# Kernel optimization log

Measured on AMD Instinct MI355X. Metric: run time of the kernel, lower is better.

Reference implementation:

```python
import jax, jax.numpy as jnp
import numpy as np

B, S, DIN = 1, 2048, 4096
H, KV, DH = 32, 8, 128          # num_heads, num_kv_groups, head_dim
G = H // KV                      # group_size


def setup_inputs() -> dict:
    key = jax.random.key(0)
    ks = jax.random.split(key, 6)
    input_tensor = jax.random.normal(ks[0], (B, S, DIN), jnp.float32)
    # boolean mask: True = masked out. Causal upper-triangular mask.
    attention_mask = jnp.triu(jnp.ones((S, S), bool), k=1)[None, None]
    # RoPE tables (context_len, head_dim), rotate-half layout
    inv_freq = 1.0 / (10000.0 ** (jnp.arange(0, DH, 2, dtype=jnp.float32) / DH))
    ang = jnp.arange(S, dtype=jnp.float32)[:, None] * inv_freq[None, :]  # (S, DH/2)
    ang = jnp.concatenate([ang, ang], axis=-1)                            # (S, DH)
    cos, sin = jnp.cos(ang), jnp.sin(ang)
    scale = 0.02
    Wq = jax.random.normal(ks[1], (DIN, H * DH), jnp.float32) * scale
    Wk = jax.random.normal(ks[2], (DIN, KV * DH), jnp.float32) * scale
    Wv = jax.random.normal(ks[3], (DIN, KV * DH), jnp.float32) * scale
    Wo = jax.random.normal(ks[4], (H * DH, DIN), jnp.float32) * scale
    return {"input_tensor": input_tensor, "attention_mask": attention_mask,
            "cos": cos, "sin": sin, "Wq": Wq, "Wk": Wk, "Wv": Wv, "Wo": Wo}


def _rope(t, cos, sin):
    # t: (B, heads, S, DH); cos/sin: (S, DH)
    t1, t2 = jnp.split(t, 2, axis=-1)
    rot = jnp.concatenate([-t2, t1], axis=-1)
    return t * cos[None, None] + rot * sin[None, None]


def reference(input_tensor, attention_mask, cos, sin, Wq, Wk, Wv, Wo):
    b, s, _ = input_tensor.shape
    q = (input_tensor @ Wq).reshape(b, s, H, DH).transpose(0, 2, 1, 3)   # (B,H,S,DH)
    k = (input_tensor @ Wk).reshape(b, s, KV, DH).transpose(0, 2, 1, 3)  # (B,KV,S,DH)
    v = (input_tensor @ Wv).reshape(b, s, KV, DH).transpose(0, 2, 1, 3)
    q = _rope(q, cos, sin)
    k = _rope(k, cos, sin)
    # GQA: duplicate each kv head across its group of query heads
    k = jnp.repeat(k, G, axis=1)  # (B,H,S,DH)
    v = jnp.repeat(v, G, axis=1)
    scores = jnp.einsum('bhqd,bhkd->bhqk', q, k)
    scores = jnp.where(attention_mask, -jnp.inf, scores)
    weights = jax.nn.softmax(scores / np.float32(np.sqrt(DH)), axis=-1)
    ctx = jnp.einsum('bhqk,bhkd->bhqd', weights, v)
    ctx = ctx.transpose(0, 2, 1, 3).reshape(b, s, H * DH)
    return ctx @ Wo
```

## Files before the change

kernel.cpp:

```cpp
#include <hip/hip_runtime.h>
#include <hip/hip_bf16.h>
#include <stdint.h>
#include <stddef.h>

typedef __attribute__((ext_vector_type(8))) short bf16x8;
typedef __attribute__((ext_vector_type(8))) unsigned short u16x8;
typedef __attribute__((ext_vector_type(4))) float f32x4;
typedef __attribute__((ext_vector_type(16))) float f32x16;

#define MFMA16(a, b, c) __builtin_amdgcn_mfma_f32_16x16x32_bf16((a), (b), (c), 0, 0, 0)
#define MFMA32(a, b, c) __builtin_amdgcn_mfma_f32_32x32x16_bf16((a), (b), (c), 0, 0, 0)

__device__ __forceinline__ unsigned short f2b(float f) {
  union { float f; unsigned u; } v; v.f = f;
  unsigned r = v.u + 0x7fffu + ((v.u >> 16) & 1u);
  return (unsigned short)(r >> 16);
}
__device__ __forceinline__ float b2f(unsigned short h) {
  union { unsigned u; float f; } v; v.u = ((unsigned)h) << 16;
  return v.f;
}

__device__ __forceinline__ void gload_lds16(const void* g, void* l) {
  __builtin_amdgcn_global_load_lds((const __attribute__((address_space(1))) void*)g,
                                   (__attribute__((address_space(3))) void*)l, 16, 0, 0);
}

__global__ void k_transpose_qkv(const float* __restrict__ Wq, const float* __restrict__ Wk,
                                const float* __restrict__ Wv, unsigned short* __restrict__ out) {
  __shared__ float tile[64][65];
  const int kb = blockIdx.x * 64;
  const int nbg = blockIdx.y * 64;
  const float* src; int srcN, nb;
  if (nbg < 4096)      { src = Wq; srcN = 4096; nb = nbg; }
  else if (nbg < 5120) { src = Wk; srcN = 1024; nb = nbg - 4096; }
  else                 { src = Wv; srcN = 1024; nb = nbg - 5120; }
  const int t = threadIdx.x;
  const int c4 = (t & 15) * 4;
  const int rr = t >> 4;
#pragma unroll
  for (int i = 0; i < 4; ++i) {
    int r = rr + i * 16;
    float4 v = *reinterpret_cast<const float4*>(src + (size_t)(kb + r) * srcN + nb + c4);
    tile[r][c4 + 0] = v.x; tile[r][c4 + 1] = v.y;
    tile[r][c4 + 2] = v.z; tile[r][c4 + 3] = v.w;
  }
  __syncthreads();
#pragma unroll
  for (int i = 0; i < 4; ++i) {
    int n = rr + i * 16;
    ushort4 w;
    w.x = f2b(tile[c4 + 0][n]); w.y = f2b(tile[c4 + 1][n]);
    w.z = f2b(tile[c4 + 2][n]); w.w = f2b(tile[c4 + 3][n]);
    *reinterpret_cast<ushort4*>(out + (size_t)(nbg + n) * 4096 + kb + c4) = w;
  }
}

__global__ void k_transpose_f32_bf16(const float* __restrict__ in,
                                     unsigned short* __restrict__ out,
                                     int K, int N) {
  __shared__ float tile[64][65];
  const int kb = blockIdx.x * 64;
  const int nb = blockIdx.y * 64;
  const int t = threadIdx.x;
  const int c4 = (t & 15) * 4;
  const int rr = t >> 4;
#pragma unroll
  for (int i = 0; i < 4; ++i) {
    int r = rr + i * 16;
    float4 v = *reinterpret_cast<const float4*>(in + (size_t)(kb + r) * N + nb + c4);
    tile[r][c4 + 0] = v.x; tile[r][c4 + 1] = v.y;
    tile[r][c4 + 2] = v.z; tile[r][c4 + 3] = v.w;
  }
  __syncthreads();
#pragma unroll
  for (int i = 0; i < 4; ++i) {
    int n = rr + i * 16;
    ushort4 w;
    w.x = f2b(tile[c4 + 0][n]); w.y = f2b(tile[c4 + 1][n]);
    w.z = f2b(tile[c4 + 2][n]); w.w = f2b(tile[c4 + 3][n]);
    *reinterpret_cast<ushort4*>(out + (size_t)(nb + n) * K + kb + c4) = w;
  }
}

__global__ void k_f32_to_bf16(const float* __restrict__ in, unsigned short* __restrict__ out) {
  size_t i = ((size_t)blockIdx.x * blockDim.x + threadIdx.x) * 4;
  float4 v = *reinterpret_cast<const float4*>(in + i);
  ushort4 w; w.x = f2b(v.x); w.y = f2b(v.y); w.z = f2b(v.z); w.w = f2b(v.w);
  *reinterpret_cast<ushort4*>(out + i) = w;
}

template <bool OUT_F32>
__global__ void __launch_bounds__(256, 2)
k_gemm(const unsigned short* __restrict__ A, const unsigned short* __restrict__ Bt,
       void* __restrict__ C, int M, int N, int K) {
  __shared__ unsigned short As[128 * 64];
  __shared__ unsigned short Bs[128 * 64];
  const int nbm = M >> 7;
  const int per = ((M >> 7) * (N >> 7)) >> 3;
  const int wg  = (blockIdx.x & 7) * per + (blockIdx.x >> 3);
  const int m0 = (wg % nbm) * 128;
  const int n0 = (wg / nbm) * 128;
  const int tid = threadIdx.x;
  const int lane = tid & 63;
  const int w = tid >> 6;
  const int wr = w >> 1, wc = w & 1;
  const int cl = lane & 15, rg = lane >> 4;

  f32x4 acc[4][4] = {};

  for (int k0 = 0; k0 < K; k0 += 64) {
#pragma unroll
    for (int i = 0; i < 4; ++i) {
      int c = i * 256 + tid;
      int row = c >> 3;
      int sc = ((c & 7) * 8) ^ ((row & 7) * 8);
      gload_lds16(A + (size_t)(m0 + row) * K + k0 + sc, As + c * 8);
    }
#pragma unroll
    for (int i = 0; i < 4; ++i) {
      int c = i * 256 + tid;
      int row = c >> 3;
      int sc = ((c & 7) * 8) ^ ((row & 7) * 8);
      gload_lds16(Bt + (size_t)(n0 + row) * K + k0 + sc, Bs + c * 8);
    }
    __syncthreads();
    bf16x8 a[4][2], b[4][2];
#pragma unroll
    for (int mi = 0; mi < 4; ++mi) {
      int row = wr * 64 + mi * 16 + cl;
      int swz = (row & 7) << 4;
#pragma unroll
      for (int ks = 0; ks < 2; ++ks)
        a[mi][ks] = *reinterpret_cast<const bf16x8*>(
            (const char*)As + ((row * 128 + (ks * 32 + rg * 8) * 2) ^ swz));
    }
#pragma unroll
    for (int ni = 0; ni < 4; ++ni) {
      int row = wc * 64 + ni * 16 + cl;
      int swz = (row & 7) << 4;
#pragma unroll
      for (int ks = 0; ks < 2; ++ks)
        b[ni][ks] = *reinterpret_cast<const bf16x8*>(
            (const char*)Bs + ((row * 128 + (ks * 32 + rg * 8) * 2) ^ swz));
    }
#pragma unroll
    for (int ks = 0; ks < 2; ++ks)
#pragma unroll
      for (int mi = 0; mi < 4; ++mi)
#pragma unroll
        for (int ni = 0; ni < 4; ++ni)
          acc[mi][ni] = MFMA16(a[mi][ks], b[ni][ks], acc[mi][ni]);
    __syncthreads();
  }
#pragma unroll
  for (int mi = 0; mi < 4; ++mi)
#pragma unroll
    for (int ni = 0; ni < 4; ++ni) {
      int row = m0 + wr * 64 + mi * 16 + rg * 4;
      int col = n0 + wc * 64 + ni * 16 + cl;
#pragma unroll
      for (int r = 0; r < 4; ++r) {
        float v = acc[mi][ni][r];
        if (OUT_F32) ((float*)C)[(size_t)(row + r) * N + col] = v;
        else         ((unsigned short*)C)[(size_t)(row + r) * N + col] = f2b(v);
      }
    }
}

__global__ void k_rope(const unsigned short* __restrict__ Cpre,
                       const float* __restrict__ cosb, const float* __restrict__ sinb,
                       unsigned short* __restrict__ Qr, unsigned short* __restrict__ Kr) {
  const int s = blockIdx.x;
  const int hh = blockIdx.y * 2 + (threadIdx.x >> 7);
  const int d = threadIdx.x & 127;
  const int col = (hh < 32) ? hh * 128 + d : 4096 + (hh - 32) * 128 + d;
  float t = b2f(Cpre[(size_t)s * 6144 + col]);
  const int dp = (d < 64) ? d + 64 : d - 64;
  float tp = b2f(Cpre[(size_t)s * 6144 + (col - d + dp)]);
  float rot = (d < 64) ? -tp : tp;
  float o = t * cosb[s * 128 + d] + rot * sinb[s * 128 + d];
  if (hh < 32) {
    Qr[((size_t)hh * 2048 + s) * 128 + d] = f2b(o * 0.08838834764831845f);
  } else {
    Kr[((size_t)(hh - 32) * 2048 + s) * 128 + d] = f2b(o);
  }
}

__global__ void k_transpose_v(const unsigned short* __restrict__ Cpre,
                              unsigned short* __restrict__ Vt) {
  __shared__ unsigned short tile[64][72];
  const int sb = blockIdx.x * 64;
  const int db = blockIdx.y * 64;
  const int kv = blockIdx.z;
  const int t = threadIdx.x;
#pragma unroll
  for (int i = 0; i < 2; ++i) {
    int sl = i * 32 + (t >> 3);
    int d8 = (t & 7) * 8;
    const unsigned short* src = Cpre + (size_t)(sb + sl) * 6144 + 5120 + kv * 128 + db + d8;
    ushort4 v0 = *reinterpret_cast<const ushort4*>(src);
    ushort4 v1 = *reinterpret_cast<const ushort4*>(src + 4);
    *reinterpret_cast<ushort4*>(&tile[sl][d8]) = v0;
    *reinterpret_cast<ushort4*>(&tile[sl][d8 + 4]) = v1;
  }
  __syncthreads();
#pragma unroll
  for (int i = 0; i < 2; ++i) {
    int dl = i * 32 + (t >> 3);
    int s8 = (t & 7) * 8;
    ushort4 w0, w1;
    w0.x = tile[s8 + 0][dl]; w0.y = tile[s8 + 1][dl]; w0.z = tile[s8 + 2][dl]; w0.w = tile[s8 + 3][dl];
    w1.x = tile[s8 + 4][dl]; w1.y = tile[s8 + 5][dl]; w1.z = tile[s8 + 6][dl]; w1.w = tile[s8 + 7][dl];
    unsigned short* dst = Vt + ((size_t)kv * 128 + db + dl) * 2048 + sb + s8;
    *reinterpret_cast<ushort4*>(dst) = w0;
    *reinterpret_cast<ushort4*>(dst + 4) = w1;
  }
}

__global__ void __launch_bounds__(256, 2)
k_attn(const unsigned short* __restrict__ Qr, const unsigned short* __restrict__ Kr,
       const unsigned short* __restrict__ Vt, unsigned short* __restrict__ ctx) {
  __shared__ unsigned short Ks[2][64 * 128];
  __shared__ unsigned short Vs[2][128 * 64];
  const int bid = blockIdx.x;
  const int kv = bid & 7;
  const int hd = kv * 4 + ((bid >> 3) & 3);
  const int qb = 15 - (bid >> 5);
  const int q0 = qb * 128;
  const int tid = threadIdx.x;
  const int l = tid & 63;
  const int w = tid >> 6;
  const int i5 = l & 31;
  const int h  = l >> 5;
  const int qg = q0 + w * 16 + (i5 & 15) + (i5 >> 4) * 64;

  const char* Kbase = (const char*)(Kr + (size_t)kv * 2048 * 128);
  const char* Vbase = (const char*)(Vt + (size_t)kv * 128 * 2048);

  bf16x8 qf[8];
#pragma unroll
  for (int s = 0; s < 8; ++s)
    qf[s] = *reinterpret_cast<const bf16x8*>(
        Qr + ((size_t)hd * 2048 + qg) * 128 + s * 16 + h * 8);

  f32x16 po[4] = {};
  float mrow = -1e30f, lrow = 0.f;

  const int krow = tid >> 4;
  const int kcol = (tid & 15) * 16;
  const int vrow = tid >> 3;
  const int vcol = (tid & 7) * 16;

#define STAGE_KV(JT, BUF)                                                      \
  {                                                                            \
    _Pragma("unroll")                                                          \
    for (int ii = 0; ii < 4; ++ii) {                                           \
      int row = ii * 16 + krow;                                                \
      gload_lds16(Kbase + (size_t)((JT) * 64 + row) * 256 +                    \
                      (kcol ^ ((row & 7) << 4)),                               \
                  (char*)Ks[BUF] + row * 256 + kcol);                          \
    }                                                                          \
    _Pragma("unroll")                                                          \
    for (int ii = 0; ii < 4; ++ii) {                                           \
      int row = ii * 32 + vrow;                                                \
      gload_lds16(Vbase + (size_t)row * 4096 + (JT) * 128 +                    \
                      (vcol ^ ((row & 7) << 4)),                               \
                  (char*)Vs[BUF] + row * 128 + vcol);                          \
    }                                                                          \
  }

  STAGE_KV(0, 0)

  const int jmax = 2 * qb + 2;
  for (int j = 0; j < jmax; ++j) {
    const int cur = j & 1;
    const int jn = (j + 1 < jmax) ? j + 1 : j;
    STAGE_KV(jn, cur ^ 1)
    asm volatile("s_waitcnt vmcnt(8)" ::: "memory");
    __builtin_amdgcn_sched_barrier(0);
    __builtin_amdgcn_s_barrier();
    __builtin_amdgcn_sched_barrier(0);

    const unsigned short* Kc = Ks[cur];
    const unsigned short* Vc = Vs[cur];

    f32x16 sa[2] = {};
    __builtin_amdgcn_s_setprio(1);
#pragma unroll
    for (int ni = 0; ni < 2; ++ni) {
      const int row = ni * 32 + i5;
      const int swz = (row & 7) << 4;
#pragma unroll
      for (int s = 0; s < 8; ++s) {
        bf16x8 kf = *reinterpret_cast<const bf16x8*>(
            (const char*)Kc + ((row * 256 + s * 32 + h * 16) ^ swz));
        sa[ni] = MFMA32(kf, qf[s], sa[ni]);
      }
    }
    __builtin_amdgcn_s_setprio(0);

    if (j >= 2 * qb) {
#pragma unroll
      for (int ni = 0; ni < 2; ++ni) {
        const int kvb = j * 64 + ni * 32 + 4 * h;
#pragma unroll
        for (int r = 0; r < 16; ++r) {
          int kvg = kvb + (r & 3) + 8 * (r >> 2);
          if (kvg > qg) sa[ni][r] = -__builtin_inff();
        }
      }
    }

    float pmax = sa[0][0];
#pragma unroll
    for (int r = 1; r < 16; ++r) pmax = fmaxf(pmax, sa[0][r]);
#pragma unroll
    for (int r = 0; r < 16; ++r) pmax = fmaxf(pmax, sa[1][r]);
    pmax = fmaxf(pmax, __shfl_xor(pmax, 32));

    if (!__all(pmax <= mrow + 8.0f)) {
      float mnew = fmaxf(mrow, pmax);
      float sf = __expf(mrow - mnew);
#pragma unroll
      for (int d = 0; d < 4; ++d)
#pragma unroll
        for (int r = 0; r < 16; ++r) po[d][r] *= sf;
      lrow *= sf;
      mrow = mnew;
    }

    float rs = 0.f;
#pragma unroll
    for (int ni = 0; ni < 2; ++ni)
#pragma unroll
      for (int r = 0; r < 16; ++r) {
        float p = __expf(sa[ni][r] - mrow);
        sa[ni][r] = p;
        rs += p;
      }
    rs += __shfl_xor(rs, 32);
    lrow += rs;

    bf16x8 pfrag[4];
#pragma unroll
    for (int ni = 0; ni < 2; ++ni) {
      unsigned wd[8];
#pragma unroll
      for (int c = 0; c < 4; ++c)
#pragma unroll
        for (int ii = 0; ii < 2; ++ii)
          wd[c * 2 + ii] = (unsigned)f2b(sa[ni][4 * c + 2 * ii]) |
                           ((unsigned)f2b(sa[ni][4 * c + 2 * ii + 1]) << 16);
#pragma unroll
      for (int k2 = 0; k2 < 2; ++k2) {
        unsigned e0 = wd[(2 * k2) * 2 + 0], e1 = wd[(2 * k2) * 2 + 1];
        unsigned o0 = wd[(2 * k2 + 1) * 2 + 0], o1 = wd[(2 * k2 + 1) * 2 + 1];
        unsigned pe0 = (unsigned)__shfl_xor((int)e0, 32);
        unsigned pe1 = (unsigned)__shfl_xor((int)e1, 32);
        unsigned po0 = (unsigned)__shfl_xor((int)o0, 32);
        unsigned po1 = (unsigned)__shfl_xor((int)o1, 32);
        union { unsigned u[4]; bf16x8 v; } uu;
        uu.u[0] = h ? po0 : e0;
        uu.u[1] = h ? po1 : e1;
        uu.u[2] = h ? o0 : pe0;
        uu.u[3] = h ? o1 : pe1;
        pfrag[ni * 2 + k2] = uu.v;
      }
    }

    __builtin_amdgcn_s_setprio(1);
#pragma unroll
    for (int d = 0; d < 4; ++d) {
      const int row0 = d * 32 + i5;
      const int swz = (row0 & 7) << 4;
#pragma unroll
      for (int ks = 0; ks < 4; ++ks) {
        bf16x8 vf = *reinterpret_cast<const bf16x8*>(
            (const char*)Vc + ((row0 * 128 + ks * 32 + h * 16) ^ swz));
        po[d] = MFMA32(vf, pfrag[ks], po[d]);
      }
    }
    __builtin_amdgcn_s_setprio(0);

    __builtin_amdgcn_sched_barrier(0);
    __builtin_amdgcn_s_barrier();
    __builtin_amdgcn_sched_barrier(0);
  }
#undef STAGE_KV

  const float inv = 1.0f / lrow;
#pragma unroll
  for (int d = 0; d < 4; ++d)
#pragma unroll
    for (int c = 0; c < 4; ++c) {
      ushort4 st;
      st.x = f2b(po[d][4 * c + 0] * inv);
      st.y = f2b(po[d][4 * c + 1] * inv);
      st.z = f2b(po[d][4 * c + 2] * inv);
      st.w = f2b(po[d][4 * c + 3] * inv);
      *reinterpret_cast<ushort4*>(
          ctx + (size_t)qg * 4096 + hd * 128 + d * 32 + 8 * c + 4 * h) = st;
    }
}

extern "C" void kernel_launch(void* const* d_in, const int* in_sizes, int n_in,
                              void* d_out, int out_size, void* d_ws, size_t ws_size,
                              hipStream_t stream) {
  const float* X    = (const float*)d_in[0];
  const float* cosb = (const float*)d_in[2];
  const float* sinb = (const float*)d_in[3];
  const float* Wq   = (const float*)d_in[4];
  const float* Wk   = (const float*)d_in[5];
  const float* Wv   = (const float*)d_in[6];
  const float* Wo   = (const float*)d_in[7];

  char* ws = (char*)d_ws;
  unsigned short* WT   = (unsigned short*)(ws + 0);
  unsigned short* Xb   = (unsigned short*)(ws + 50331648ull);
  unsigned short* Cpre = (unsigned short*)(ws + 67108864ull);
  unsigned short* Qr   = (unsigned short*)(ws + 92274688ull);
  unsigned short* Kr   = (unsigned short*)(ws + 109051904ull);
  unsigned short* Vt   = (unsigned short*)(ws + 113246208ull);
  unsigned short* ctx  = Cpre;

  k_transpose_qkv<<<dim3(64, 96), 256, 0, stream>>>(Wq, Wk, Wv, WT);
  k_f32_to_bf16<<<8192, 256, 0, stream>>>(X, Xb);

  k_gemm<false><<<768, 256, 0, stream>>>(Xb, WT, Cpre, 2048, 6144, 4096);

  k_rope<<<dim3(2048, 20), 256, 0, stream>>>(Cpre, cosb, sinb, Qr, Kr);
  k_transpose_v<<<dim3(32, 2, 8), 256, 0, stream>>>(Cpre, Vt);

  k_transpose_f32_bf16<<<dim3(64, 64), 256, 0, stream>>>(Wo, WT, 4096, 4096);

  k_attn<<<512, 256, 0, stream>>>(Qr, Kr, Vt, ctx);

  k_gemm<true><<<512, 256, 0, stream>>>(ctx, WT, d_out, 2048, 4096, 4096);
}
```

Before: 323.2 us.

## Double-buffer GEMM LDS tiles to overlap global loads with MFMA

New measurement: 358.8 us. +11.0%, slower.

```diff
diff --git a/kernel.cpp b/kernel.cpp
--- a/kernel.cpp
+++ b/kernel.cpp
@@ -94,8 +94,8 @@
 __global__ void __launch_bounds__(256, 2)
 k_gemm(const unsigned short* __restrict__ A, const unsigned short* __restrict__ Bt,
        void* __restrict__ C, int M, int N, int K) {
-  __shared__ unsigned short As[128 * 64];
-  __shared__ unsigned short Bs[128 * 64];
+  __shared__ unsigned short As[2][128 * 64];
+  __shared__ unsigned short Bs[2][128 * 64];
   const int nbm = M >> 7;
   const int per = ((M >> 7) * (N >> 7)) >> 3;
   const int wg  = (blockIdx.x & 7) * per + (blockIdx.x >> 3);
@@ -109,22 +109,38 @@
 
   f32x4 acc[4][4] = {};
 
-  for (int k0 = 0; k0 < K; k0 += 64) {
-#pragma unroll
-    for (int i = 0; i < 4; ++i) {
-      int c = i * 256 + tid;
-      int row = c >> 3;
-      int sc = ((c & 7) * 8) ^ ((row & 7) * 8);
-      gload_lds16(A + (size_t)(m0 + row) * K + k0 + sc, As + c * 8);
-    }
-#pragma unroll
-    for (int i = 0; i < 4; ++i) {
-      int c = i * 256 + tid;
-      int row = c >> 3;
-      int sc = ((c & 7) * 8) ^ ((row & 7) * 8);
-      gload_lds16(Bt + (size_t)(n0 + row) * K + k0 + sc, Bs + c * 8);
-    }
-    __syncthreads();
+#define GSTAGE(T, BUF)                                                         \
+  {                                                                            \
+    _Pragma("unroll")                                                          \
+    for (int i = 0; i < 4; ++i) {                                              \
+      int c = i * 256 + tid;                                                   \
+      int row = c >> 3;                                                        \
+      int sc = ((c & 7) * 8) ^ ((row & 7) * 8);                                \
+      gload_lds16(A + (size_t)(m0 + row) * K + (size_t)(T) * 64 + sc,          \
+                  As[BUF] + c * 8);                                            \
+    }                                                                          \
+    _Pragma("unroll")                                                          \
+    for (int i = 0; i < 4; ++i) {                                              \
+      int c = i * 256 + tid;                                                   \
+      int row = c >> 3;                                                        \
+      int sc = ((c & 7) * 8) ^ ((row & 7) * 8);                                \
+      gload_lds16(Bt + (size_t)(n0 + row) * K + (size_t)(T) * 64 + sc,         \
+                  Bs[BUF] + c * 8);                                            \
+    }                                                                          \
+  }
+
+  GSTAGE(0, 0)
+
+  const int nt = K >> 6;
+  for (int t = 0; t < nt; ++t) {
+    const int cur = t & 1;
+    const int tn = (t + 1 < nt) ? t + 1 : t;
+    GSTAGE(tn, cur ^ 1)
+    asm volatile("s_waitcnt vmcnt(8)" ::: "memory");
+    __builtin_amdgcn_sched_barrier(0);
+    __builtin_amdgcn_s_barrier();
+    __builtin_amdgcn_sched_barrier(0);
+
     bf16x8 a[4][2], b[4][2];
 #pragma unroll
     for (int mi = 0; mi < 4; ++mi) {
@@ -133,7 +149,7 @@
 #pragma unroll
       for (int ks = 0; ks < 2; ++ks)
         a[mi][ks] = *reinterpret_cast<const bf16x8*>(
-            (const char*)As + ((row * 128 + (ks * 32 + rg * 8) * 2) ^ swz));
+            (const char*)As[cur] + ((row * 128 + (ks * 32 + rg * 8) * 2) ^ swz));
     }
 #pragma unroll
     for (int ni = 0; ni < 4; ++ni) {
@@ -142,8 +158,9 @@
 #pragma unroll
       for (int ks = 0; ks < 2; ++ks)
         b[ni][ks] = *reinterpret_cast<const bf16x8*>(
-            (const char*)Bs + ((row * 128 + (ks * 32 + rg * 8) * 2) ^ swz));
-    }
+            (const char*)Bs[cur] + ((row * 128 + (ks * 32 + rg * 8) * 2) ^ swz));
+    }
+    __builtin_amdgcn_s_setprio(1);
 #pragma unroll
     for (int ks = 0; ks < 2; ++ks)
 #pragma unroll
@@ -151,8 +168,14 @@
 #pragma unroll
         for (int ni = 0; ni < 4; ++ni)
           acc[mi][ni] = MFMA16(a[mi][ks], b[ni][ks], acc[mi][ni]);
-    __syncthreads();
-  }
+    __builtin_amdgcn_s_setprio(0);
+
+    __builtin_amdgcn_sched_barrier(0);
+    __builtin_amdgcn_s_barrier();
+    __builtin_amdgcn_sched_barrier(0);
+  }
+#undef GSTAGE
+
 #pragma unroll
   for (int mi = 0; mi < 4; ++mi)
 #pragma unroll
```
